# Kernel tuning notes

Measured on AMD Instinct MI355X. Metric: run time of the kernel, lower is better.

The kernel has to match this reference:

```python
import jax, jax.numpy as jnp
import numpy as np

HEADS, DH, M_LAND, PINV_ITERS, LN_EPS = 8, 64, 256, 6, 1e-5


def layer_norm(x, g, b):
    mu = x.mean(-1, keepdims=True)
    var = ((x - mu) ** 2).mean(-1, keepdims=True)
    return (x - mu) * jax.lax.rsqrt(var + LN_EPS) * g + b


def moore_penrose_pinv(x, iters=PINV_ITERS):
    # x: (h, m, m). Iterative Newton-Schulz style pinv (lucidrains).
    abs_x = jnp.abs(x)
    col = abs_x.sum(-1)
    row = abs_x.sum(-2)
    z = jnp.swapaxes(x, -1, -2) / (jnp.max(col) * jnp.max(row))
    I = jnp.eye(x.shape[-1], dtype=x.dtype)
    for _ in range(iters):
        xz = x @ z
        z = 0.25 * z @ (13.0 * I - xz @ (15.0 * I - xz @ (7.0 * I - xz)))
    return z


def nystrom_attention(x, qkv_w, out_w, out_b, res_w):
    # x: (n, dim). No mask, eval mode (dropout off).
    n, dim = x.shape
    pad = (-n) % M_LAND
    xp = jnp.pad(x, ((pad, 0), (0, 0)))  # pad at sequence START, as in original
    n_p = n + pad
    l = n_p // M_LAND  # tokens per landmark
    qkv = xp @ qkv_w  # (n_p, 3*h*dh)
    q, k, v = jnp.split(qkv, 3, axis=-1)
    split = lambda t: t.reshape(n_p, HEADS, DH).transpose(1, 0, 2)  # (h, n_p, dh)
    q, k, v = split(q), split(k), split(v)
    q = q * (DH ** -0.5)
    q_l = q.reshape(HEADS, M_LAND, l, DH).mean(axis=2)  # (h, m, dh)
    k_l = k.reshape(HEADS, M_LAND, l, DH).mean(axis=2)
    sim1 = jnp.einsum('hid,hjd->hij', q, k_l)    # (h, n_p, m)
    sim2 = jnp.einsum('hid,hjd->hij', q_l, k_l)  # (h, m, m)
    sim3 = jnp.einsum('hid,hjd->hij', q_l, k)    # (h, m, n_p)
    a1 = jax.nn.softmax(sim1, axis=-1)
    a2 = jax.nn.softmax(sim2, axis=-1)
    a3 = jax.nn.softmax(sim3, axis=-1)
    a2_inv = moore_penrose_pinv(a2)
    out = a1 @ (a2_inv @ (a3 @ v))  # (h, n_p, dh)
    # residual depthwise conv over sequence dim, kernel 33, per head
    res = jax.lax.conv_general_dilated(
        v[None], res_w, (1, 1), ((16, 16), (0, 0)),
        feature_group_count=HEADS, dimension_numbers=('NCHW', 'OIHW', 'NCHW'))[0]
    out = out + res
    out = out.transpose(1, 0, 2).reshape(n_p, HEADS * DH)
    out = out @ out_w + out_b
    return out[-n:]  # drop the leading pad


def ppeg(x, w7, b7, w5, b5, w3, b3, H, W):
    cls_tok, feat = x[0], x[1:]
    C = feat.shape[1]
    img = feat.T.reshape(1, C, H, W)
    def dw(w, b, p):
        y = jax.lax.conv_general_dilated(
            img, w, (1, 1), ((p, p), (p, p)),
            feature_group_count=C, dimension_numbers=('NCHW', 'OIHW', 'NCHW'))
        return y + b.reshape(1, C, 1, 1)
    out = img + dw(w7, b7, 3) + dw(w5, b5, 2) + dw(w3, b3, 1)
    out = out[0].reshape(C, H * W).T
    return jnp.concatenate([cls_tok[None], out], axis=0)


def forward(h, fc1_w, fc1_b, cls_token, l1_ln_g, l1_ln_b, l1_qkv_w, l1_out_w, l1_out_b, l1_res_w,
            conv7_w, conv7_b, conv5_w, conv5_b, conv3_w, conv3_b,
            l2_ln_g, l2_ln_b, l2_qkv_w, l2_out_w, l2_out_b, l2_res_w,
            norm_g, norm_b, fc2_w, fc2_b):
    x = jax.nn.relu(h @ fc1_w + fc1_b)  # (N, 512)
    N = x.shape[0]
    Hs = Ws = int(np.ceil(np.sqrt(N)))  # N chosen perfect square -> add_length == 0
    x = jnp.concatenate([cls_token, x], axis=0)  # (N+1, 512)
    x = x + nystrom_attention(layer_norm(x, l1_ln_g, l1_ln_b), l1_qkv_w, l1_out_w, l1_out_b, l1_res_w)
    x = ppeg(x, conv7_w, conv7_b, conv5_w, conv5_b, conv3_w, conv3_b, Hs, Ws)
    x = x + nystrom_attention(layer_norm(x, l2_ln_g, l2_ln_b), l2_qkv_w, l2_out_w, l2_out_b, l2_res_w)
    x = layer_norm(x, norm_g, norm_b)[0]  # cls token readout
    return x @ fc2_w + fc2_b  # (n_classes,)


def setup_inputs() -> dict:
    key = jax.random.key(0)
    ks = jax.random.split(key, 16)
    nrm = lambda k, s, sc=0.02: jax.random.normal(k, s, jnp.float32) * sc
    D = 512
    return {
        'h': jax.random.normal(ks[0], (16384, 2048), jnp.float32),
        'fc1_w': nrm(ks[1], (2048, D)), 'fc1_b': jnp.zeros((D,), jnp.float32),
        'cls_token': nrm(ks[2], (1, D), 1.0),
        'l1_ln_g': jnp.ones((D,), jnp.float32), 'l1_ln_b': jnp.zeros((D,), jnp.float32),
        'l1_qkv_w': nrm(ks[3], (D, 3 * D)),
        'l1_out_w': nrm(ks[4], (D, D)), 'l1_out_b': jnp.zeros((D,), jnp.float32),
        'l1_res_w': nrm(ks[5], (HEADS, 1, 33, 1), 0.05),
        'conv7_w': nrm(ks[6], (D, 1, 7, 7), 0.05), 'conv7_b': jnp.zeros((D,), jnp.float32),
        'conv5_w': nrm(ks[7], (D, 1, 5, 5), 0.05), 'conv5_b': jnp.zeros((D,), jnp.float32),
        'conv3_w': nrm(ks[8], (D, 1, 3, 3), 0.05), 'conv3_b': jnp.zeros((D,), jnp.float32),
        'l2_ln_g': jnp.ones((D,), jnp.float32), 'l2_ln_b': jnp.zeros((D,), jnp.float32),
        'l2_qkv_w': nrm(ks[9], (D, 3 * D)),
        'l2_out_w': nrm(ks[10], (D, D)), 'l2_out_b': jnp.zeros((D,), jnp.float32),
        'l2_res_w': nrm(ks[11], (HEADS, 1, 33, 1), 0.05),
        'norm_g': jnp.ones((D,), jnp.float32), 'norm_b': jnp.zeros((D,), jnp.float32),
        'fc2_w': nrm(ks[12], (D, 2)), 'fc2_b': jnp.zeros((2,), jnp.float32),
    }


def reference(h, fc1_w, fc1_b, cls_token, l1_ln_g, l1_ln_b, l1_qkv_w, l1_out_w, l1_out_b, l1_res_w,
              conv7_w, conv7_b, conv5_w, conv5_b, conv3_w, conv3_b,
              l2_ln_g, l2_ln_b, l2_qkv_w, l2_out_w, l2_out_b, l2_res_w,
              norm_g, norm_b, fc2_w, fc2_b):
    return forward(h, fc1_w, fc1_b, cls_token, l1_ln_g, l1_ln_b, l1_qkv_w, l1_out_w, l1_out_b, l1_res_w,
                   conv7_w, conv7_b, conv5_w, conv5_b, conv3_w, conv3_b,
                   l2_ln_g, l2_ln_b, l2_qkv_w, l2_out_w, l2_out_b, l2_res_w,
                   norm_g, norm_b, fc2_w, fc2_b)
```

## Files before the change

kernel.cpp:

```cpp
#include <hip/hip_runtime.h>
#include <cstddef>

#define NROWS 16385
#define NPAD  16640
#define PADT  255
#define DIM   512
#define HEADS 8
#define DH    64
#define NL    256
#define LCH   65
#define LCHUNK 52
#define KCH   320
#define SLACK 24
#define LDST  40

typedef short bf16x8 __attribute__((ext_vector_type(8)));
typedef float f32x4  __attribute__((ext_vector_type(4)));

__device__ __forceinline__ float wsum(float v){
#pragma unroll
  for (int o = 32; o; o >>= 1) v += __shfl_xor(v, o);
  return v;
}
__device__ __forceinline__ float wmax(float v){
#pragma unroll
  for (int o = 32; o; o >>= 1) v = fmaxf(v, __shfl_xor(v, o));
  return v;
}
__device__ __forceinline__ float red16max(float v){
  v = fmaxf(v, __shfl_xor(v, 1));
  v = fmaxf(v, __shfl_xor(v, 2));
  v = fmaxf(v, __shfl_xor(v, 4));
  v = fmaxf(v, __shfl_xor(v, 8));
  return v;
}
__device__ __forceinline__ float red16sum(float v){
  v += __shfl_xor(v, 1);
  v += __shfl_xor(v, 2);
  v += __shfl_xor(v, 4);
  v += __shfl_xor(v, 8);
  return v;
}

__device__ __forceinline__ void split2(float x, unsigned short &h, unsigned short &l){
  unsigned ux = __float_as_uint(x);
  unsigned rh = (ux + 0x7FFFu + ((ux >> 16) & 1u)) >> 16;
  h = (unsigned short)rh;
  float fh = __uint_as_float(rh << 16);
  float r = x - fh;
  unsigned ur = __float_as_uint(r);
  unsigned rl = (ur + 0x7FFFu + ((ur >> 16) & 1u)) >> 16;
  l = (unsigned short)rl;
}
__device__ __forceinline__ float bf2f(unsigned short h){
  return __uint_as_float((unsigned)h << 16);
}

__global__ __launch_bounds__(256) void gemm64_sp_kernel(
    const unsigned short* __restrict__ Ah, const unsigned short* __restrict__ Al,
    const unsigned short* __restrict__ Bth, const unsigned short* __restrict__ Btl,
    const unsigned short* __restrict__ IBh, const unsigned short* __restrict__ IBl,
    float* __restrict__ Cf,
    unsigned short* __restrict__ Crh, unsigned short* __restrict__ Crl,
    unsigned short* __restrict__ Cth, unsigned short* __restrict__ Ctl,
    int M, int N, int K, long sA, long sB, long sC,
    float alpha, float ib)
{
  size_t zo = (size_t)blockIdx.z;
  Ah  += zo*sA; Al  += zo*sA;
  Bth += zo*sB; Btl += zo*sB;
  if (IBh){ IBh += zo*sA; IBl += zo*sA; }
  if (Cf)  Cf  += zo*sC;
  if (Crh){ Crh += zo*sC; Crl += zo*sC; }
  if (Cth){ Cth += zo*sC; Ctl += zo*sC; }
  __shared__ unsigned short LAh[64*LDST], LAl[64*LDST], LBh[64*LDST], LBl[64*LDST];
  const int t = threadIdx.x;
  const int wid = t >> 6, lane = t & 63;
  const int wr = wid >> 1, wc = wid & 1;
  const int l15 = lane & 15, kb = lane >> 4;
  const int bm = blockIdx.y << 6, bn = blockIdx.x << 6;
  const int r4 = t >> 2, kc = (t & 3) << 3;
  f32x4 acc[2][2];
#pragma unroll
  for (int i=0;i<2;++i)
#pragma unroll
    for (int j=0;j<2;++j) acc[i][j] = (f32x4){0.f,0.f,0.f,0.f};

  for (int k0 = 0; k0 < K; k0 += 32){
    __syncthreads();
    {
      int lo = r4*LDST + kc;
      *(uint4*)&LAh[lo] = *(const uint4*)&Ah[(size_t)(bm+r4)*K + k0 + kc];
      *(uint4*)&LAl[lo] = *(const uint4*)&Al[(size_t)(bm+r4)*K + k0 + kc];
      *(uint4*)&LBh[lo] = *(const uint4*)&Bth[(size_t)(bn+r4)*K + k0 + kc];
      *(uint4*)&LBl[lo] = *(const uint4*)&Btl[(size_t)(bn+r4)*K + k0 + kc];
    }
    __syncthreads();
    bf16x8 ah[2], al[2], bh[2], bl[2];
#pragma unroll
    for (int r=0;r<2;++r){
      int off = (wr*32 + r*16 + l15)*LDST + kb*8;
      ah[r] = *(const bf16x8*)&LAh[off];
      al[r] = *(const bf16x8*)&LAl[off];
    }
#pragma unroll
    for (int c2=0;c2<2;++c2){
      int off = (wc*32 + c2*16 + l15)*LDST + kb*8;
      bh[c2] = *(const bf16x8*)&LBh[off];
      bl[c2] = *(const bf16x8*)&LBl[off];
    }
#pragma unroll
    for (int r=0;r<2;++r)
#pragma unroll
      for (int c2=0;c2<2;++c2){
        acc[r][c2] = __builtin_amdgcn_mfma_f32_16x16x32_bf16(ah[r], bh[c2], acc[r][c2], 0,0,0);
        acc[r][c2] = __builtin_amdgcn_mfma_f32_16x16x32_bf16(ah[r], bl[c2], acc[r][c2], 0,0,0);
        acc[r][c2] = __builtin_amdgcn_mfma_f32_16x16x32_bf16(al[r], bh[c2], acc[r][c2], 0,0,0);
      }
  }
#pragma unroll
  for (int r=0;r<2;++r){
#pragma unroll
    for (int c2=0;c2<2;++c2){
      int col = bn + wc*32 + c2*16 + l15;
      int rb  = bm + wr*32 + r*16 + kb*4;
      float v[4];
#pragma unroll
      for (int e=0;e<4;++e){
        float x = acc[r][c2][e];
        if (ib != 0.f){
          size_t io = (size_t)(rb+e)*K + col;
          float ibv = bf2f(IBh[io]) + bf2f(IBl[io]);
          x = alpha*(ib*ibv - x);
        } else {
          x = alpha*x;
        }
        v[e] = x;
      }
      if (Cf){
#pragma unroll
        for (int e=0;e<4;++e) Cf[(size_t)(rb+e)*N + col] = v[e];
      }
      if (Crh){
#pragma unroll
        for (int e=0;e<4;++e){
          unsigned short hh, ll;
          split2(v[e], hh, ll);
          Crh[(size_t)(rb+e)*N + col] = hh;
          Crl[(size_t)(rb+e)*N + col] = ll;
        }
      }
      if (Cth){
        unsigned short h4[4], l4[4];
#pragma unroll
        for (int e=0;e<4;++e) split2(v[e], h4[e], l4[e]);
        uint2 uh, ul;
        uh.x = (unsigned)h4[0] | ((unsigned)h4[1]<<16);
        uh.y = (unsigned)h4[2] | ((unsigned)h4[3]<<16);
        ul.x = (unsigned)l4[0] | ((unsigned)l4[1]<<16);
        ul.y = (unsigned)l4[2] | ((unsigned)l4[3]<<16);
        *(uint2*)&Cth[(size_t)col*M + rb] = uh;
        *(uint2*)&Ctl[(size_t)col*M + rb] = ul;
      }
    }
  }
}

// ... 93 lines not shown
  const int l15 = lane & 15, kb = lane >> 4;
  const int sr = t >> 1, sc0 = (t & 1) << 4;
  f32x4 acc[4][4];
#pragma unroll
  for (int i=0;i<4;++i)
#pragma unroll
    for (int j=0;j<4;++j) acc[i][j] = (f32x4){0.f,0.f,0.f,0.f};

  for (int k0 = 0; k0 < K; k0 += 32){
    __syncthreads();
    {
      const float* ap = A + (size_t)(bm + sr)*K + k0 + sc0;
      float va[16];
      *(float4*)&va[0]  = ((const float4*)ap)[0];
      *(float4*)&va[4]  = ((const float4*)ap)[1];
      *(float4*)&va[8]  = ((const float4*)ap)[2];
      *(float4*)&va[12] = ((const float4*)ap)[3];
      int lo = sr*LDST + sc0;
      unsigned* dh = (unsigned*)&LAh[lo];
      unsigned* dl = (unsigned*)&LAl[lo];
#pragma unroll
      for (int q=0;q<8;++q){
        unsigned short h0,l0,h1,l1;
        split2(va[2*q],   h0, l0);
        split2(va[2*q+1], h1, l1);
        dh[q] = (unsigned)h0 | ((unsigned)h1 << 16);
        dl[q] = (unsigned)l0 | ((unsigned)l1 << 16);
      }
      size_t gb = (size_t)(bn + sr)*K + k0 + sc0;
      uint4 b0 = *(const uint4*)(BTh + gb);
      uint4 b1 = *(const uint4*)(BTh + gb + 8);
      uint4 b2 = *(const uint4*)(BTl + gb);
      uint4 b3 = *(const uint4*)(BTl + gb + 8);
      *(uint4*)&LBh[lo] = b0; *(uint4*)&LBh[lo+8] = b1;
      *(uint4*)&LBl[lo] = b2; *(uint4*)&LBl[lo+8] = b3;
    }
    __syncthreads();
    bf16x8 ah[4], al[4], bh[4], bl[4];
#pragma unroll
    for (int ai=0; ai<4; ++ai){
      int off = (wr*64 + ai*16 + l15)*LDST + kb*8;
      ah[ai] = *(const bf16x8*)&LAh[off];
      al[ai] = *(const bf16x8*)&LAl[off];
    }
#pragma unroll
    for (int bj=0; bj<4; ++bj){
      int off = (wc*64 + bj*16 + l15)*LDST + kb*8;
      bh[bj] = *(const bf16x8*)&LBh[off];
      bl[bj] = *(const bf16x8*)&LBl[off];
    }
#pragma unroll
    for (int ai=0; ai<4; ++ai)
#pragma unroll
      for (int bj=0; bj<4; ++bj){
        acc[ai][bj] = __builtin_amdgcn_mfma_f32_16x16x32_bf16(ah[ai], bh[bj], acc[ai][bj], 0,0,0);
        acc[ai][bj] = __builtin_amdgcn_mfma_f32_16x16x32_bf16(ah[ai], bl[bj], acc[ai][bj], 0,0,0);
        acc[ai][bj] = __builtin_amdgcn_mfma_f32_16x16x32_bf16(al[ai], bh[bj], acc[ai][bj], 0,0,0);
      }
  }
#pragma unroll
  for (int ai=0; ai<4; ++ai){
#pragma unroll
    for (int bj=0; bj<4; ++bj){
      int col = bn + wc*64 + bj*16 + l15;
      float bv = bias ? bias[col] : 0.f;
#pragma unroll
      for (int r=0; r<4; ++r){
        int row = bm + wr*64 + ai*16 + kb*4 + r;
        float v = acc[ai][bj][r] + bv;
        if (relu) v = fmaxf(v, 0.f);
        C[(size_t)row*N + col] = v;
      }
    }
  }
}

__global__ void wt_split_T_kernel(const float* __restrict__ W,
                                  unsigned short* __restrict__ BTh,
                                  unsigned short* __restrict__ BTl, int K, int N)
{
  int idx = blockIdx.x*256 + threadIdx.x;
  if (idx >= N*K) return;
  int n = idx / K, k = idx - n*K;
  unsigned short h, l;
  split2(W[(size_t)k*N + n], h, l);
  BTh[idx] = h; BTl[idx] = l;
}

__global__ void att_split_kernel(const float* __restrict__ ATT,
                                 unsigned short* __restrict__ Ah,
                                 unsigned short* __restrict__ Al)
{
  size_t i4 = (size_t)blockIdx.x*256 + threadIdx.x;
  size_t e = i4*4;
  int row = (int)(e >> 9);
  float4 v = make_float4(0.f,0.f,0.f,0.f);
  if (row < NROWS) v = *(const float4*)(ATT + (size_t)PADT*DIM + e);
  unsigned short h0,l0,h1,l1,h2,l2,h3,l3;
  split2(v.x,h0,l0); split2(v.y,h1,l1); split2(v.z,h2,l2); split2(v.w,h3,l3);
  uint2 uh, ul;
  uh.x = (unsigned)h0 | ((unsigned)h1<<16); uh.y = (unsigned)h2 | ((unsigned)h3<<16);
  ul.x = (unsigned)l0 | ((unsigned)l1<<16); ul.y = (unsigned)l2 | ((unsigned)l3<<16);
  *(uint2*)(Ah + e) = uh;
  *(uint2*)(Al + e) = ul;
}

__global__ __launch_bounds__(256) void ln_pad_sb_kernel(
    const float* __restrict__ X, const float* __restrict__ g,
    const float* __restrict__ b, unsigned short* __restrict__ Yh,
    unsigned short* __restrict__ Yl)
{
  int p = blockIdx.x;
  int t = threadIdx.x;
  size_t base = (size_t)p*DIM;
  if (p < PADT){
    Yh[base+t] = 0; Yh[base+t+256] = 0;
    Yl[base+t] = 0; Yl[base+t+256] = 0;
    return;
  }
  const float* xr = X + (size_t)(p-PADT)*DIM;
  float x0 = xr[t], x1 = xr[t+256];
  float s = x0 + x1, sq = x0*x0 + x1*x1;
  s = wsum(s); sq = wsum(sq);
  __shared__ float rs[4], rq[4];
  if ((t&63)==0){ rs[t>>6]=s; rq[t>>6]=sq; }
  __syncthreads();
  float S = rs[0]+rs[1]+rs[2]+rs[3];
  float SQ = rq[0]+rq[1]+rq[2]+rq[3];
  float mu = S * (1.f/DIM);
  float var = SQ * (1.f/DIM) - mu*mu;
  float r = rsqrtf(var + 1e-5f);
  float y0 = (x0-mu)*r*g[t]     + b[t];
  float y1 = (x1-mu)*r*g[t+256] + b[t+256];
  unsigned short h, l;
  split2(y0, h, l); Yh[base+t] = h;     Yl[base+t] = l;
  split2(y1, h, l); Yh[base+t+256] = h; Yl[base+t+256] = l;
}

__global__ void landmarks_kernel(const float* __restrict__ QKV,
                                 float* __restrict__ QL, float* __restrict__ KL)
{
  int m = blockIdx.x, h = blockIdx.y, d = threadIdx.x;
  float sq = 0.f, sk = 0.f;
  const float* base = QKV + (size_t)(m*LCH)*1536 + (h<<6) + d;
  for (int j = 0; j < LCH; ++j){
    sq += base[0];
    sk += base[512];
    base += 1536;
  }
  QL[(((h<<8)+m)<<6) + d] = sq * (0.125f/65.f);
  KL[(((h<<8)+m)<<6) + d] = sk * (1.f/65.f);
}

__global__ __launch_bounds__(256) void sim2_kernel(
    const float* __restrict__ QL, const float* __restrict__ KL, float* __restrict__ A2)
{
  int m = blockIdx.x, h = blockIdx.y, n = threadIdx.x;
  __shared__ float ql[64];
  __shared__ float red[4];
  if (n < 64) ql[n] = QL[(((h<<8)+m)<<6) + n];
  __syncthreads();
  const float* kl = KL + (size_t)(((h<<8)+n)<<6);
  float s = 0.f;
#pragma unroll
  for (int d=0; d<64; ++d) s += ql[d]*kl[d];
  float mx = wmax(s);
  if ((n&63)==0) red[n>>6] = mx;
  __syncthreads();
  mx = fmaxf(fmaxf(red[0],red[1]), fmaxf(red[2],red[3]));
  float e = __expf(s - mx);
  float sm = wsum(e);
  __syncthreads();
  if ((n&63)==0) red[n>>6] = sm;
  __syncthreads();
  sm = red[0]+red[1]+red[2]+red[3];
  A2[((size_t)((h<<8)+m)<<8) + n] = e/sm;
}

__global__ void crsum_kernel(const float* __restrict__ A2, float* __restrict__ CR)
{
  int b = blockIdx.x, t = threadIdx.x;
  float v;
  if (b < 2048){
    v = fabsf(A2[((size_t)b<<8) + t]);
  } else {
    int r = b - 2048;
    int h = r >> 8, n = r & 255;
    v = fabsf(A2[((size_t)h<<16) + (t<<8) + n]);
  }
  v = wsum(v);
  __shared__ float red[4];
  if ((t&63)==0) red[t>>6]=v;
  __syncthreads();
  if (t==0) CR[b] = red[0]+red[1]+red[2]+red[3];
}
__global__ void maxprod_kernel(const float* __restrict__ CR, float* __restrict__ SCAL)
{
  int t = threadIdx.x;
  float mc = -3e38f, mr = -3e38f;
  for (int i=t; i<2048; i+=256){ mc = fmaxf(mc, CR[i]); mr = fmaxf(mr, CR[2048+i]); }
  mc = wmax(mc); mr = wmax(mr);
  __shared__ float rc[4], rr[4];
  if ((t&63)==0){ rc[t>>6]=mc; rr[t>>6]=mr; }
  __syncthreads();
  if (t==0){
    float a = fmaxf(fmaxf(rc[0],rc[1]),fmaxf(rc[2],rc[3]));
    float b = fmaxf(fmaxf(rr[0],rr[1]),fmaxf(rr[2],rr[3]));
    SCAL[0] = 1.f/(a*b);
  }
}

__global__ void tsplit_kernel(const float* __restrict__ A2, const float* __restrict__ SCAL,
                              unsigned short* __restrict__ A2h, unsigned short* __restrict__ A2l,
                              unsigned short* __restrict__ Zrh, unsigned short* __restrict__ Zrl,
                              unsigned short* __restrict__ Zth, unsigned short* __restrict__ Ztl)
{
  int idx = blockIdx.x*256 + threadIdx.x;
  int h = idx >> 16, rem = idx & 65535, m = rem >> 8, n = rem & 255;
  float a = A2[idx];
  unsigned short hh, ll;
  split2(a, hh, ll);
  A2h[idx] = hh; A2l[idx] = ll;
  float z = a * SCAL[0];
  split2(z, hh, ll);
  Zth[idx] = hh; Ztl[idx] = ll;
  size_t rmo = ((size_t)h<<16) + (n<<8) + m;
  Zrh[rmo] = hh; Zrl[rmo] = ll;
}

__global__ __launch_bounds__(256) void lattn2_kernel(
    const float* __restrict__ QKV, const float* __restrict__ QL,
    float* __restrict__ PACC, float* __restrict__ PML)
{
  const int c = blockIdx.x, lg = blockIdx.y, h = blockIdx.z;
  const int t = threadIdx.x, tx = t & 15, ty = t >> 4;
  __shared__ float QLs[64][68], KtsPs[64][68], Vs[64][68];
  {
    int r = t >> 2, c0 = (t & 3) << 4;
    const float* src = QL + (((size_t)((h << 8) + (lg << 6) + r)) << 6) + c0;
#pragma unroll
    for (int q = 0; q < 4; ++q)
      *(float4*)&QLs[r][c0 + (q<<2)] = ((const float4*)src)[q];
  }
  float M[4], L[4], acc[4][4];
#pragma unroll
  for (int i = 0; i < 4; ++i){
    M[i] = -3e38f; L[i] = 0.f;
#pragma unroll
    for (int j = 0; j < 4; ++j) acc[i][j] = 0.f;
  }
  const int key = t & 63, kd0 = (t >> 6) << 4;
  const int vr = t >> 2, vc = (t & 3) << 4;
  for (int s = 0; s < 5; ++s){
    const int j0 = c * KCH + (s << 6);
    __syncthreads();
    {
      const float* kp = QKV + (size_t)(j0 + key) * 1536 + 512 + (h << 6) + kd0;
#pragma unroll
      for (int q = 0; q < 4; ++q){
        float4 kv = ((const float4*)kp)[q];
        KtsPs[kd0 + (q<<2) + 0][key] = kv.x;
        KtsPs[kd0 + (q<<2) + 1][key] = kv.y;
        KtsPs[kd0 + (q<<2) + 2][key] = kv.z;
        KtsPs[kd0 + (q<<2) + 3][key] = kv.w;
      }
      const float* vp = QKV + (size_t)(j0 + vr) * 1536 + 1024 + (h << 6) + vc;
#pragma unroll
      for (int q = 0; q < 4; ++q)
        *(float4*)&Vs[vr][vc + (q<<2)] = ((const float4*)vp)[q];
    }
    __syncthreads();
    float sv[4][4];
#pragma unroll
    for (int i=0;i<4;++i)
#pragma unroll
      for (int j=0;j<4;++j) sv[i][j] = 0.f;
    for (int d = 0; d < 64; d += 4){
      float a[4][4], b[4][4];
#pragma unroll
      for (int i = 0; i < 4; ++i)
        *(float4*)a[i] = *(const float4*)&QLs[(ty<<2)+i][d];
#pragma unroll
      for (int dd = 0; dd < 4; ++dd)
        *(float4*)b[dd] = *(const float4*)&KtsPs[d+dd][tx<<2];
#pragma unroll
      for (int i = 0; i < 4; ++i)
#pragma unroll
        for (int dd = 0; dd < 4; ++dd){
          float av = a[i][dd];
#pragma unroll
          for (int j = 0; j < 4; ++j) sv[i][j] += av * b[dd][j];
        }
    }
#pragma unroll
    for (int i = 0; i < 4; ++i){
      float rm = fmaxf(fmaxf(sv[i][0], sv[i][1]), fmaxf(sv[i][2], sv[i][3]));
      rm = red16max(rm);
      float Mn = fmaxf(M[i], rm);
      float sc = __expf(M[i] - Mn);
      float rs = 0.f;
#pragma unroll
      for (int j = 0; j < 4; ++j){
        float p = __expf(sv[i][j] - Mn);
        sv[i][j] = p; rs += p;
      }
      rs = red16sum(rs);
      L[i] = L[i] * sc + rs;
      M[i] = Mn;
#pragma unroll
      for (int j = 0; j < 4; ++j) acc[i][j] *= sc;
    }
    __syncthreads();
#pragma unroll
    for (int i = 0; i < 4; ++i)
      *(float4*)&KtsPs[(ty<<2)+i][tx<<2] = *(float4*)sv[i];
    for (int k = 0; k < 64; k += 4){
      float a[4][4], b[4][4];
#pragma unroll
      for (int i = 0; i < 4; ++i)
        *(float4*)a[i] = *(const float4*)&KtsPs[(ty<<2)+i][k];
#pragma unroll
      for (int kk = 0; kk < 4; ++kk)
        *(float4*)b[kk] = *(const float4*)&Vs[k+kk][tx<<2];
#pragma unroll
      for (int i = 0; i < 4; ++i)
#pragma unroll
        for (int kk = 0; kk < 4; ++kk){
          float av = a[i][kk];
#pragma unroll
          for (int j = 0; j < 4; ++j) acc[i][j] += av * b[kk][j];
        }
    }
  }
  size_t base = (size_t)(c * 8 + h) * 256 + (lg << 6) + (ty << 2);
#pragma unroll
  for (int i = 0; i < 4; ++i)
    *(float4*)&PACC[(base + i) * 64 + (tx << 2)] = *(float4*)acc[i];
  if (tx == 0){
#pragma unroll
    for (int i = 0; i < 4; ++i){
      PML[(base + i) * 2 + 0] = M[i];
      PML[(base + i) * 2 + 1] = L[i];
    }
  }
}

__global__ void lattn_combine_kernel(const float* __restrict__ PACC,
                                     const float* __restrict__ PML,
                                     unsigned short* __restrict__ TMth,
                                     unsigned short* __restrict__ TMtl)
{
  int hm = blockIdx.x, d = threadIdx.x;
  int h = hm >> 8, m = hm & 255;
  float Mg = -3e38f;
#pragma unroll
  for (int c = 0; c < LCHUNK; ++c){
    size_t b = ((size_t)(c * 8 + h) * 256 + m) * 2;
    Mg = fmaxf(Mg, PML[b]);
  }
  float Sg = 0.f, o = 0.f;
#pragma unroll 4
  for (int c = 0; c < LCHUNK; ++c){
    size_t b = ((size_t)(c * 8 + h) * 256 + m) * 2;
    float e = __expf(PML[b] - Mg);
    Sg += PML[b+1] * e;
    o += PACC[((size_t)(c * 8 + h) * 256 + m) * 64 + d] * e;
  }
  unsigned short hh, ll;
  split2(o / Sg, hh, ll);
  size_t off = (size_t)h*16384 + (size_t)d*256 + m;
  TMth[off] = hh; TMtl[off] = ll;
}

__global__ __launch_bounds__(256) void attn2_kernel(
    const float* __restrict__ QKV, const float* __restrict__ KL,
    const float* __restrict__ BM, float* __restrict__ ATT)
{
  const int h = blockIdx.y;
  const int t = threadIdx.x;
  const int d0 = (t & 3) << 4;
  const int rp = t >> 2;
  const int row0 = blockIdx.x*128 + rp*2;
  __shared__ float KLs[64][64];
  __shared__ float BMs[64][64];
  float q[2][16], acc[2][16];
  float m[2] = {-3e38f, -3e38f}, l[2] = {0.f, 0.f};
#pragma unroll
  for (int r = 0; r < 2; ++r){
    int qr = row0 + r; if (qr > NROWS-1) qr = NROWS-1;
    const float4* qp = (const float4*)(QKV + (size_t)(PADT+qr)*1536 + (h<<6) + d0);
#pragma unroll
    for (int i = 0; i < 4; ++i){
      float4 v = qp[i];
      q[r][4*i+0]=v.x*0.125f; q[r][4*i+1]=v.y*0.125f;
      q[r][4*i+2]=v.z*0.125f; q[r][4*i+3]=v.w*0.125f;
      acc[r][4*i+0]=0.f; acc[r][4*i+1]=0.f; acc[r][4*i+2]=0.f; acc[r][4*i+3]=0.f;
    }
  }
  for (int c = 0; c < 4; ++c){
    __syncthreads();
    {
      const float4* ks = (const float4*)(KL + (((size_t)(h<<8) + (c<<6))<<6));
      const float4* bs = (const float4*)(BM + ((size_t)h<<14) + ((size_t)(c<<6)<<6));
      float4* kd = (float4*)&KLs[0][0];
      float4* bd = (float4*)&BMs[0][0];
      for (int i = t; i < 1024; i += 256){ kd[i] = ks[i]; bd[i] = bs[i]; }
    }
    __syncthreads();
#pragma unroll 1
    for (int n = 0; n < 64; ++n){
      const float* klr = &KLs[n][d0];
      float sA = 0.f, sB = 0.f;
#pragma unroll
      for (int j = 0; j < 16; ++j){
        sA = fmaf(q[0][j], klr[j], sA);
        sB = fmaf(q[1][j], klr[j], sB);
      }
      sA += __shfl_xor(sA, 1); sA += __shfl_xor(sA, 2);
      sB += __shfl_xor(sB, 1); sB += __shfl_xor(sB, 2);
      const float* bmr = &BMs[n][d0];
      if (sA > m[0]){
        float sc = __expf(m[0] - sA); l[0] *= sc;
#pragma unroll
        for (int j = 0; j < 16; ++j) acc[0][j] *= sc;
        m[0] = sA;
      }
      if (sB > m[1]){
        float sc = __expf(m[1] - sB); l[1] *= sc;
#pragma unroll
        for (int j = 0; j < 16; ++j) acc[1][j] *= sc;
        m[1] = sB;
      }
      float pA = __expf(sA - m[0]); l[0] += pA;
      float pB = __expf(sB - m[1]); l[1] += pB;
#pragma unroll
      for (int j = 0; j < 16; ++j){
        acc[0][j] = fmaf(pA, bmr[j], acc[0][j]);
        acc[1][j] = fmaf(pB, bmr[j], acc[1][j]);
      }
    }
  }
#pragma unroll
  for (int r = 0; r < 2; ++r){
    int row = row0 + r;
    if (row < NROWS){
      float inv = 1.f/l[r];
      float* op = ATT + (size_t)(PADT+row)*DIM + (h<<6) + d0;
#pragma unroll
      for (int j = 0; j < 16; j += 4){
        float4 o;
        o.x=acc[r][j]*inv; o.y=acc[r][j+1]*inv; o.z=acc[r][j+2]*inv; o.w=acc[r][j+3]*inv;
        *(float4*)(op+j) = o;
      }
    }
  }
}

__global__ void zero_slack_kernel(float* __restrict__ QKV)
{
  int i = blockIdx.x*256 + threadIdx.x;
  QKV[(size_t)NPAD*1536 + i] = 0.f;
}

__global__ __launch_bounds__(256) void convres2_kernel(
    const float* __restrict__ QKV, const float* __restrict__ rw,
    float* __restrict__ ATT)
{
  const int t = threadIdx.x;
  const int c = blockIdx.y*256 + t;
  const int i0 = PADT + (blockIdx.x << 2);
  const int h = c >> 6;
  float w[33];
#pragma unroll
  for (int k=0;k<33;++k) w[k] = rw[h*33 + k];
  float acc[4] = {0.f,0.f,0.f,0.f};
  const float* vbase = QKV + (size_t)(i0-16)*1536 + 1024 + c;
#pragma unroll
  for (int rr=0; rr<36; ++rr){
    float v = vbase[(size_t)rr*1536];
#pragma unroll
    for (int k=0;k<4;++k){
      int tap = rr - k;
      if (tap >= 0 && tap <= 32) acc[k] += w[tap]*v;
    }
  }
#pragma unroll
  for (int k=0;k<4;++k){
    int i = i0 + k;
    if (i < NPAD) ATT[(size_t)i*DIM + c] += acc[k];
  }
}

__global__ void pad_kernel(const float* __restrict__ X, float* __restrict__ PIM)
{
  int r = blockIdx.x;
  int c = blockIdx.y*256 + threadIdx.x;
  int py = r / 134, px = r - py*134;
  float v = 0.f;
  if (py>=3 && py<131 && px>=3 && px<131)
    v = X[(size_t)(1 + (py-3)*128 + (px-3))*512 + c];
  PIM[(size_t)r*512 + c] = v;
}

__global__ void wtrans_kernel(const float* __restrict__ w7, const float* __restrict__ w5,
                              const float* __restrict__ w3, float* __restrict__ W7T,
                              float* __restrict__ W5T, float* __restrict__ W3T)
{
  int i = blockIdx.x;
  int c = blockIdx.y*256 + threadIdx.x;
  if (i < 49)      W7T[i*512+c]      = w7[c*49+i];
  else if (i < 74) W5T[(i-49)*512+c] = w5[c*25+(i-49)];
  else             W3T[(i-74)*512+c] = w3[c*9+(i-74)];
}

__global__ __launch_bounds__(256) void ppeg2_kernel(
    const float* __restrict__ PIM, const float* __restrict__ W7T,
    const float* __restrict__ W5T, const float* __restrict__ W3T,
    const float* __restrict__ b7, const float* __restrict__ b5,
    const float* __restrict__ b3, float* __restrict__ X2)
{
  const int t = threadIdx.x;
  const int c = blockIdx.z*256 + t;
  const int x = blockIdx.x;
  const int y0 = blockIdx.y << 2;
  float w7r[49], w5r[25], w3r[9];
#pragma unroll
  for (int i=0;i<49;++i) w7r[i] = W7T[i*512 + c];
#pragma unroll
  for (int i=0;i<25;++i) w5r[i] = W5T[i*512 + c];
#pragma unroll
  for (int i=0;i<9;++i)  w3r[i] = W3T[i*512 + c];
  const float bsum = b7[c] + b5[c] + b3[c];
  float acc[4] = {bsum, bsum, bsum, bsum};
  const float* base = PIM + ((size_t)(y0*134 + x))*512 + c;
#pragma unroll
  for (int rr=0; rr<10; ++rr){
#pragma unroll
    for (int cc=0; cc<7; ++cc){
      float v = base[(size_t)(rr*134 + cc)*512];
#pragma unroll
      for (int k=0;k<4;++k){
        const int dy = rr - k - 3, dx = cc - 3;
        if (dy >= -3 && dy <= 3){
          acc[k] += w7r[(dy+3)*7 + (dx+3)] * v;
          if (dy >= -2 && dy <= 2 && dx >= -2 && dx <= 2)
            acc[k] += w5r[(dy+2)*5 + (dx+2)] * v;
          if (dy >= -1 && dy <= 1 && dx >= -1 && dx <= 1)
            acc[k] += w3r[(dy+1)*3 + (dx+1)] * v;
          if (dy == 0 && dx == 0) acc[k] += v;
        }
      }
    }
  }
#pragma unroll
  for (int k=0;k<4;++k)
    X2[(size_t)(1 + (y0+k)*128 + x)*512 + c] = acc[k];
}

__global__ void copy_row_kernel(const float* __restrict__ src, float* __restrict__ dst)
{
  dst[threadIdx.x] = src[threadIdx.x];
}

__global__ void final_kernel(const float* __restrict__ X, const float* __restrict__ g,
                             const float* __restrict__ b, const float* __restrict__ fw,
                             const float* __restrict__ fb, float* __restrict__ out)
{
  int t = threadIdx.x;
  float x0 = X[t], x1 = X[t+256];
  float s = x0 + x1, sq = x0*x0 + x1*x1;
  s = wsum(s); sq = wsum(sq);
  __shared__ float rs[4], rq[4];
  if ((t&63)==0){ rs[t>>6]=s; rq[t>>6]=sq; }
  __syncthreads();
  float S = rs[0]+rs[1]+rs[2]+rs[3];
  float SQ = rq[0]+rq[1]+rq[2]+rq[3];
  float mu = S*(1.f/DIM);
  float var = SQ*(1.f/DIM) - mu*mu;
  float r = rsqrtf(var + 1e-5f);
  float n0 = (x0-mu)*r*g[t]     + b[t];
  float n1 = (x1-mu)*r*g[t+256] + b[t+256];
  float p0 = n0*fw[t*2]   + n1*fw[(t+256)*2];
  float p1 = n0*fw[t*2+1] + n1*fw[(t+256)*2+1];
  p0 = wsum(p0); p1 = wsum(p1);
  __shared__ float r0[4], r1[4];
  if ((t&63)==0){ r0[t>>6]=p0; r1[t>>6]=p1; }
  __syncthreads();
  if (t==0){
    out[0] = r0[0]+r0[1]+r0[2]+r0[3] + fb[0];
    out[1] = r1[0]+r1[1]+r1[2]+r1[3] + fb[1];
  }
}

struct Bufs {
  float *Y, *QKV, *QL, *KL, *A2, *CR, *SCAL, *BM, *PACC, *PML, *W7T, *W5T, *W3T;
  unsigned short *Yh, *Yl, *ATh, *ATl, *qBTh, *qBTl, *oBTh, *oBTl, *fBTh, *fBTl;
  unsigned short *A2h, *A2l, *XZrh, *XZrl, *XZth, *XZtl, *Wth, *Wtl, *W2th, *W2tl;
  unsigned short *Z0rh, *Z0rl, *Z0th, *Z0tl, *Z1rh, *Z1rl, *Z1th, *Z1tl;
  unsigned short *TMth, *TMtl;
};

static void attention_layer(float* X, const float* ln_g, const float* ln_b,
                            const float* qkv_w, const float* out_w, const float* out_b,
                            const float* res_w, Bufs& bf, hipStream_t stream)
{
  const long SP = 65536;
  wt_split_T_kernel<<<(1536*512)/256, 256, 0, stream>>>(qkv_w, bf.qBTh, bf.qBTl, 512, 1536);
  wt_split_T_kernel<<<(512*512)/256, 256, 0, stream>>>(out_w, bf.oBTh, bf.oBTl, 512, 512);
  ln_pad_sb_kernel<<<NPAD, 256, 0, stream>>>(X, ln_g, ln_b, bf.Yh, bf.Yl);
  gemm_sb_kernel<<<dim3(12,130),256,0,stream>>>(bf.Yh, bf.Yl, bf.qBTh, bf.qBTl,
      nullptr, bf.QKV, NPAD, 1536, 512, 0);
  landmarks_kernel<<<dim3(NL,HEADS),64,0,stream>>>(bf.QKV, bf.QL, bf.KL);
  sim2_kernel<<<dim3(NL,HEADS),256,0,stream>>>(bf.QL, bf.KL, bf.A2);
  crsum_kernel<<<4096,256,0,stream>>>(bf.A2, bf.CR);
  maxprod_kernel<<<1,256,0,stream>>>(bf.CR, bf.SCAL);
  tsplit_kernel<<<2048,256,0,stream>>>(bf.A2, bf.SCAL, bf.A2h, bf.A2l,
      bf.Z0rh, bf.Z0rl, bf.Z0th, bf.Z0tl);
  unsigned short *Zarh=bf.Z0rh, *Zarl=bf.Z0rl, *Zath=bf.Z0th, *Zatl=bf.Z0tl;
  unsigned short *Zbrh=bf.Z1rh, *Zbrl=bf.Z1rl, *Zbth=bf.Z1th, *Zbtl=bf.Z1tl;
  for (int it = 0; it < 6; ++it){
    gemm64_sp_kernel<<<dim3(4,4,8),256,0,stream>>>(bf.A2h, bf.A2l, Zath, Zatl,
        nullptr, nullptr, nullptr, bf.XZrh, bf.XZrl, bf.XZth, bf.XZtl,
        256,256,256, SP,SP,SP, 1.f, 0.f);
    gemm64_sp_kernel<<<dim3(4,4,8),256,0,stream>>>(bf.XZrh, bf.XZrl, bf.XZth, bf.XZtl,
        bf.XZrh, bf.XZrl, nullptr, nullptr, nullptr, bf.Wth, bf.Wtl,
        256,256,256, SP,SP,SP, 1.f, 7.f);
    gemm64_sp_kernel<<<dim3(4,4,8),256,0,stream>>>(bf.XZrh, bf.XZrl, bf.Wth, bf.Wtl,
        bf.XZrh, bf.XZrl, nullptr, nullptr, nullptr, bf.W2th, bf.W2tl,
        256,256,256, SP,SP,SP, 1.f, 15.f);
    gemm64_sp_kernel<<<dim3(4,4,8),256,0,stream>>>(Zarh, Zarl, bf.W2th, bf.W2tl,
        Zarh, Zarl, nullptr, Zbrh, Zbrl, Zbth, Zbtl,
        256,256,256, SP,SP,SP, 0.25f, 13.f);
    unsigned short* tp;
    tp=Zarh; Zarh=Zbrh; Zbrh=tp;  tp=Zarl; Zarl=Zbrl; Zbrl=tp;
    tp=Zath; Zath=Zbth; Zbth=tp;  tp=Zatl; Zatl=Zbtl; Zbtl=tp;
  }
  lattn2_kernel<<<dim3(LCHUNK,4,HEADS),256,0,stream>>>(bf.QKV, bf.QL, bf.PACC, bf.PML);
  lattn_combine_kernel<<<2048,64,0,stream>>>(bf.PACC, bf.PML, bf.TMth, bf.TMtl);
  gemm64_sp_kernel<<<dim3(1,4,8),256,0,stream>>>(Zarh, Zarl, bf.TMth, bf.TMtl,
      nullptr, nullptr, bf.BM, nullptr, nullptr, nullptr, nullptr,
      256,64,256, SP, 16384L, 16384L, 1.f, 0.f);
  float* ATT = bf.Y;
  attn2_kernel<<<dim3(129,HEADS),256,0,stream>>>(bf.QKV, bf.KL, bf.BM, ATT);
  convres2_kernel<<<dim3(4097,2),256,0,stream>>>(bf.QKV, res_w, ATT);
  att_split_kernel<<<8256,256,0,stream>>>(ATT, bf.ATh, bf.ATl);
  gemm_sb_kernel<<<dim3(4,129),256,0,stream>>>(bf.ATh, bf.ATl, bf.oBTh, bf.oBTl,
      out_b, X, NROWS, 512, 512, 1);
}

extern "C" void kernel_launch(void* const* d_in, const int* in_sizes, int n_in,
                              void* d_out, int out_size, void* d_ws, size_t ws_size,
                              hipStream_t stream)
{
  (void)in_sizes; (void)n_in; (void)out_size; (void)ws_size;
  const float* h       = (const float*)d_in[0];
  const float* fc1_w   = (const float*)d_in[1];
  const float* fc1_b   = (const float*)d_in[2];
  const float* cls     = (const float*)d_in[3];
  const float* l1_ln_g = (const float*)d_in[4];
  const float* l1_ln_b = (const float*)d_in[5];
  const float* l1_qkv_w= (const float*)d_in[6];
  const float* l1_out_w= (const float*)d_in[7];
  const float* l1_out_b= (const float*)d_in[8];
  const float* l1_res_w= (const float*)d_in[9];
  const float* conv7_w = (const float*)d_in[10];
  const float* conv7_b = (const float*)d_in[11];
  const float* conv5_w = (const float*)d_in[12];
  const float* conv5_b = (const float*)d_in[13];
  const float* conv3_w = (const float*)d_in[14];
  const float* conv3_b = (const float*)d_in[15];
  const float* l2_ln_g = (const float*)d_in[16];
  const float* l2_ln_b = (const float*)d_in[17];
  const float* l2_qkv_w= (const float*)d_in[18];
  const float* l2_out_w= (const float*)d_in[19];
  const float* l2_out_b= (const float*)d_in[20];
  const float* l2_res_w= (const float*)d_in[21];
  const float* norm_g  = (const float*)d_in[22];
  const float* norm_b  = (const float*)d_in[23];
  const float* fc2_w   = (const float*)d_in[24];
  const float* fc2_b   = (const float*)d_in[25];

  float* ws = (float*)d_ws;
  float* X   = ws;                 ws += (size_t)NROWS*DIM;
  float* X2  = ws;                 ws += (size_t)NROWS*DIM;
  Bufs bf;
  bf.Y    = ws;                    ws += (size_t)NPAD*DIM;
  bf.QKV  = ws;                    ws += (size_t)(NPAD+SLACK)*1536;
  bf.QL   = ws;                    ws += HEADS*NL*DH;
  bf.KL   = ws;                    ws += HEADS*NL*DH;
  bf.A2   = ws;                    ws += HEADS*NL*NL;
  bf.CR   = ws;                    ws += 4096;
  bf.SCAL = ws;                    ws += 8;
  bf.BM   = ws;                    ws += HEADS*NL*DH;
  bf.PACC = ws;                    ws += (size_t)LCHUNK*HEADS*NL*DH;
  bf.PML  = ws;                    ws += (size_t)LCHUNK*HEADS*NL*2;
  bf.W7T  = ws;                    ws += 49*512;
  bf.W5T  = ws;                    ws += 25*512;
  bf.W3T  = ws;                    ws += 9*512;
  unsigned short* us = (unsigned short*)ws;
  bf.Yh   = us;                    us += (size_t)NPAD*DIM;
  bf.Yl   = us;                    us += (size_t)NPAD*DIM;
  bf.ATh  = us;                    us += (size_t)16512*DIM;
  bf.ATl  = us;                    us += (size_t)16512*DIM;
  bf.qBTh = us;                    us += 1536*512;
  bf.qBTl = us;                    us += 1536*512;
  bf.oBTh = us;                    us += 512*512;
  bf.oBTl = us;                    us += 512*512;
  bf.fBTh = us;                    us += 512*2048;
  bf.fBTl = us;                    us += 512*2048;
  const size_t PL = (size_t)HEADS*NL*NL;
  bf.A2h  = us; us += PL;  bf.A2l  = us; us += PL;
  bf.XZrh = us; us += PL;  bf.XZrl = us; us += PL;
  bf.XZth = us; us += PL;  bf.XZtl = us; us += PL;
  bf.Wth  = us; us += PL;  bf.Wtl  = us; us += PL;
  bf.W2th = us; us += PL;  bf.W2tl = us; us += PL;
  bf.Z0rh = us; us += PL;  bf.Z0rl = us; us += PL;
  bf.Z0th = us; us += PL;  bf.Z0tl = us; us += PL;
  bf.Z1rh = us; us += PL;  bf.Z1rl = us; us += PL;
  bf.Z1th = us; us += PL;  bf.Z1tl = us; us += PL;
  bf.TMth = us; us += (size_t)HEADS*NL*DH;
  bf.TMtl = us; us += (size_t)HEADS*NL*DH;
  float* PIM = bf.QKV;

  zero_slack_kernel<<<(SLACK*1536)/256, 256, 0, stream>>>(bf.QKV);
  wtrans_kernel<<<dim3(83,2),256,0,stream>>>(conv7_w, conv5_w, conv3_w,
                                             bf.W7T, bf.W5T, bf.W3T);

  wt_split_T_kernel<<<(512*2048)/256, 256, 0, stream>>>(fc1_w, bf.fBTh, bf.fBTl, 2048, 512);
  gemm_sbf_kernel<<<dim3(4,128),256,0,stream>>>(h, bf.fBTh, bf.fBTl, fc1_b, X + DIM,
      16384, 512, 2048, 1);
  copy_row_kernel<<<1,512,0,stream>>>(cls, X);

  attention_layer(X, l1_ln_g, l1_ln_b, l1_qkv_w, l1_out_w, l1_out_b, l1_res_w, bf, stream);

  pad_kernel<<<dim3(17956,2),256,0,stream>>>(X, PIM);
  ppeg2_kernel<<<dim3(128,32,2),256,0,stream>>>(PIM, bf.W7T, bf.W5T, bf.W3T,
                                                conv7_b, conv5_b, conv3_b, X2);
  copy_row_kernel<<<1,512,0,stream>>>(X, X2);

  attention_layer(X2, l2_ln_g, l2_ln_b, l2_qkv_w, l2_out_w, l2_out_b, l2_res_w, bf, stream);

  final_kernel<<<1,256,0,stream>>>(X2, norm_g, norm_b, fc2_w, fc2_b, (float*)d_out);
}
```

Baseline: 2.302 ms.

## Move attn1 landmark attention onto split-bf16 MFMA with online softmax

Replaces the scalar FP32 a1·(pinv·a3v) attention kernel with an MFMA version. Q, landmark keys and the BM matrix are split into bf16 hi/lo pairs, and three MFMAs per product emulate fp32 accuracy. A new kernel pre-splits KL, and the gemm now emits BM transposed and split. The aim is to cut the FP32 ALU cost of the per-row 256-landmark softmax-attention, at the price of extra LDS staging, more syncs and an extra small kernel launch.

```diff
diff --git a/kernel.cpp b/kernel.cpp
--- a/kernel.cpp
+++ b/kernel.cpp
@@ -13,6 +13,7 @@
 #define KCH   320
 #define SLACK 24
 #define LDST  40
+#define AST   72
 
 typedef short bf16x8 __attribute__((ext_vector_type(8)));
 typedef float f32x4  __attribute__((ext_vector_type(4)));
@@ -412,6 +413,16 @@
   KL[(((h<<8)+m)<<6) + d] = sk * (1.f/65.f);
 }
 
+__global__ void klsplit_kernel(const float* __restrict__ KL,
+                               unsigned short* __restrict__ KLh,
+                               unsigned short* __restrict__ KLl)
+{
+  int i = blockIdx.x*256 + threadIdx.x;
+  unsigned short h, l;
+  split2(KL[i], h, l);
+  KLh[i] = h; KLl[i] = l;
+}
+
 __global__ __launch_bounds__(256) void sim2_kernel(
     const float* __restrict__ QL, const float* __restrict__ KL, float* __restrict__ A2)
 {
@@ -632,86 +643,158 @@
   TMth[off] = hh; TMtl[off] = ll;
 }
 
-__global__ __launch_bounds__(256) void attn2_kernel(
-    const float* __restrict__ QKV, const float* __restrict__ KL,
-    const float* __restrict__ BM, float* __restrict__ ATT)
-{
-  const int h = blockIdx.y;
+__global__ __launch_bounds__(256) void attn3_kernel(
+    const float* __restrict__ QKV,
+    const unsigned short* __restrict__ KLh, const unsigned short* __restrict__ KLl,
+    const unsigned short* __restrict__ BMth, const unsigned short* __restrict__ BMtl,
+    float* __restrict__ ATT)
+{
+  const int qb = blockIdx.x, h = blockIdx.y;
   const int t = threadIdx.x;
-  const int d0 = (t & 3) << 4;
-  const int rp = t >> 2;
-  const int row0 = blockIdx.x*128 + rp*2;
-  __shared__ float KLs[64][64];
-  __shared__ float BMs[64][64];
-  float q[2][16], acc[2][16];
-  float m[2] = {-3e38f, -3e38f}, l[2] = {0.f, 0.f};
-#pragma unroll
-  for (int r = 0; r < 2; ++r){
-    int qr = row0 + r; if (qr > NROWS-1) qr = NROWS-1;
-    const float4* qp = (const float4*)(QKV + (size_t)(PADT+qr)*1536 + (h<<6) + d0);
-#pragma unroll
-    for (int i = 0; i < 4; ++i){
-      float4 v = qp[i];
-      q[r][4*i+0]=v.x*0.125f; q[r][4*i+1]=v.y*0.125f;
-      q[r][4*i+2]=v.z*0.125f; q[r][4*i+3]=v.w*0.125f;
-      acc[r][4*i+0]=0.f; acc[r][4*i+1]=0.f; acc[r][4*i+2]=0.f; acc[r][4*i+3]=0.f;
-    }
-  }
-  for (int c = 0; c < 4; ++c){
+  const int w = t >> 6, lane = t & 63;
+  const int l15 = lane & 15, kb = lane >> 4;
+  __shared__ unsigned short LQh[64*AST], LQl[64*AST];
+  __shared__ unsigned short LAh[64*AST], LAl[64*AST];
+  __shared__ unsigned short LPh[64*AST], LPl[64*AST];
+  {
+    int r = t >> 2, kc = (t & 3) << 4;
+    int row = qb*64 + r; if (row > NROWS-1) row = NROWS-1;
+    const float* qp = QKV + (size_t)(PADT+row)*1536 + (h<<6) + kc;
+    float va[16];
+    *(float4*)&va[0]  = ((const float4*)qp)[0];
+    *(float4*)&va[4]  = ((const float4*)qp)[1];
+    *(float4*)&va[8]  = ((const float4*)qp)[2];
+    *(float4*)&va[12] = ((const float4*)qp)[3];
+    unsigned* dh = (unsigned*)&LQh[r*AST + kc];
+    unsigned* dl = (unsigned*)&LQl[r*AST + kc];
+#pragma unroll
+    for (int q=0;q<8;++q){
+      unsigned short h0,l0,h1,l1;
+      split2(va[2*q]*0.125f,   h0, l0);
+      split2(va[2*q+1]*0.125f, h1, l1);
+      dh[q] = (unsigned)h0 | ((unsigned)h1 << 16);
+      dl[q] = (unsigned)l0 | ((unsigned)l1 << 16);
+    }
+  }
+  float m = -3e38f, l = 0.f;
+  f32x4 oacc[4];
+#pragma unroll
+  for (int i=0;i<4;++i) oacc[i] = (f32x4){0.f,0.f,0.f,0.f};
+  const int sr = t >> 2, sc0 = (t & 3) << 4;
+
+  for (int lt = 0; lt < 4; ++lt){
     __syncthreads();
     {
-      const float4* ks = (const float4*)(KL + (((size_t)(h<<8) + (c<<6))<<6));
-      const float4* bs = (const float4*)(BM + ((size_t)h<<14) + ((size_t)(c<<6)<<6));
-      float4* kd = (float4*)&KLs[0][0];
-      float4* bd = (float4*)&BMs[0][0];
-      for (int i = t; i < 1024; i += 256){ kd[i] = ks[i]; bd[i] = bs[i]; }
-    }
-    __syncthreads();
-#pragma unroll 1
-    for (int n = 0; n < 64; ++n){
-      const float* klr = &KLs[n][d0];
-      float sA = 0.f, sB = 0.f;
-#pragma unroll
-      for (int j = 0; j < 16; ++j){
-        sA = fmaf(q[0][j], klr[j], sA);
-        sB = fmaf(q[1][j], klr[j], sB);
-      }
-      sA += __shfl_xor(sA, 1); sA += __shfl_xor(sA, 2);
-      sB += __shfl_xor(sB, 1); sB += __shfl_xor(sB, 2);
-      const float* bmr = &BMs[n][d0];
-      if (sA > m[0]){
-        float sc = __expf(m[0] - sA); l[0] *= sc;
-#pragma unroll
-        for (int j = 0; j < 16; ++j) acc[0][j] *= sc;
-        m[0] = sA;
-      }
-      if (sB > m[1]){
-        float sc = __expf(m[1] - sB); l[1] *= sc;
-#pragma unroll
-        for (int j = 0; j < 16; ++j) acc[1][j] *= sc;
-        m[1] = sB;
-      }
-      float pA = __expf(sA - m[0]); l[0] += pA;
-      float pB = __expf(sB - m[1]); l[1] += pB;
-#pragma unroll
-      for (int j = 0; j < 16; ++j){
-        acc[0][j] = fmaf(pA, bmr[j], acc[0][j]);
-        acc[1][j] = fmaf(pB, bmr[j], acc[1][j]);
-      }
-    }
-  }
-#pragma unroll
-  for (int r = 0; r < 2; ++r){
-    int row = row0 + r;
-    if (row < NROWS){
-      float inv = 1.f/l[r];
-      float* op = ATT + (size_t)(PADT+row)*DIM + (h<<6) + d0;
-#pragma unroll
-      for (int j = 0; j < 16; j += 4){
-        float4 o;
-        o.x=acc[r][j]*inv; o.y=acc[r][j+1]*inv; o.z=acc[r][j+2]*inv; o.w=acc[r][j+3]*inv;
-        *(float4*)(op+j) = o;
-      }
+      size_t g = ((size_t)(h*256 + lt*64 + sr))*64 + sc0;
+      uint4 vh0 = *(const uint4*)&KLh[g];
+      uint4 vh1 = *(const uint4*)&KLh[g+8];
+      uint4 vl0 = *(const uint4*)&KLl[g];
+      uint4 vl1 = *(const uint4*)&KLl[g+8];
+      int lo = sr*AST + sc0;
+      *(uint4*)&LAh[lo]   = vh0;
+      *(uint4*)&LAh[lo+8] = vh1;
+      *(uint4*)&LAl[lo]   = vl0;
+      *(uint4*)&LAl[lo+8] = vl1;
+    }
+    __syncthreads();
+    f32x4 sacc[4];
+#pragma unroll
+    for (int i=0;i<4;++i) sacc[i] = (f32x4){0.f,0.f,0.f,0.f};
+#pragma unroll
+    for (int ks = 0; ks < 2; ++ks){
+      int qoff = (w*16 + l15)*AST + ks*32 + kb*8;
+      bf16x8 bh = *(const bf16x8*)&LQh[qoff];
+      bf16x8 bl = *(const bf16x8*)&LQl[qoff];
+#pragma unroll
+      for (int mi=0; mi<4; ++mi){
+        int aoff = (mi*16 + l15)*AST + ks*32 + kb*8;
+        bf16x8 ah = *(const bf16x8*)&LAh[aoff];
+        bf16x8 al = *(const bf16x8*)&LAl[aoff];
+        sacc[mi] = __builtin_amdgcn_mfma_f32_16x16x32_bf16(ah, bh, sacc[mi], 0,0,0);
+        sacc[mi] = __builtin_amdgcn_mfma_f32_16x16x32_bf16(ah, bl, sacc[mi], 0,0,0);
+        sacc[mi] = __builtin_amdgcn_mfma_f32_16x16x32_bf16(al, bh, sacc[mi], 0,0,0);
+      }
+    }
+    float tm = -3e38f;
+#pragma unroll
+    for (int mi=0;mi<4;++mi)
+#pragma unroll
+      for (int e=0;e<4;++e) tm = fmaxf(tm, sacc[mi][e]);
+    tm = fmaxf(tm, __shfl_xor(tm, 16));
+    tm = fmaxf(tm, __shfl_xor(tm, 32));
+    float Mn = fmaxf(m, tm);
+    float sc = __expf(m - Mn);
+    float ts = 0.f;
+    float p[4][4];
+#pragma unroll
+    for (int mi=0;mi<4;++mi)
+#pragma unroll
+      for (int e=0;e<4;++e){
+        float pv = __expf(sacc[mi][e] - Mn);
+        p[mi][e] = pv; ts += pv;
+      }
+    ts += __shfl_xor(ts, 16);
+    ts += __shfl_xor(ts, 32);
+    l = l*sc + ts;
+    m = Mn;
+#pragma unroll
+    for (int mi=0;mi<4;++mi)
+#pragma unroll
+      for (int e=0;e<4;++e) oacc[mi][e] *= sc;
+#pragma unroll
+    for (int mi=0;mi<4;++mi){
+      unsigned short h4[4], l4[4];
+#pragma unroll
+      for (int e=0;e<4;++e) split2(p[mi][e], h4[e], l4[e]);
+      uint2 uh, ul;
+      uh.x = (unsigned)h4[0] | ((unsigned)h4[1]<<16);
+      uh.y = (unsigned)h4[2] | ((unsigned)h4[3]<<16);
+      ul.x = (unsigned)l4[0] | ((unsigned)l4[1]<<16);
+      ul.y = (unsigned)l4[2] | ((unsigned)l4[3]<<16);
+      int po = (w*16 + l15)*AST + mi*16 + kb*4;
+      *(uint2*)&LPh[po] = uh;
+      *(uint2*)&LPl[po] = ul;
+    }
+    __syncthreads();
+    {
+      size_t g = ((size_t)(h*64 + sr))*256 + lt*64 + sc0;
+      uint4 vh0 = *(const uint4*)&BMth[g];
+      uint4 vh1 = *(const uint4*)&BMth[g+8];
+      uint4 vl0 = *(const uint4*)&BMtl[g];
+      uint4 vl1 = *(const uint4*)&BMtl[g+8];
+      int lo = sr*AST + sc0;
+      *(uint4*)&LAh[lo]   = vh0;
+      *(uint4*)&LAh[lo+8] = vh1;
+      *(uint4*)&LAl[lo]   = vl0;
+      *(uint4*)&LAl[lo+8] = vl1;
+    }
+    __syncthreads();
+#pragma unroll
+    for (int ks = 0; ks < 2; ++ks){
+      int poff = (w*16 + l15)*AST + ks*32 + kb*8;
+      bf16x8 pbh = *(const bf16x8*)&LPh[poff];
+      bf16x8 pbl = *(const bf16x8*)&LPl[poff];
+#pragma unroll
+      for (int mi=0; mi<4; ++mi){
+        int aoff = (mi*16 + l15)*AST + ks*32 + kb*8;
+        bf16x8 ah = *(const bf16x8*)&LAh[aoff];
+        bf16x8 al = *(const bf16x8*)&LAl[aoff];
+        oacc[mi] = __builtin_amdgcn_mfma_f32_16x16x32_bf16(ah, pbh, oacc[mi], 0,0,0);
+        oacc[mi] = __builtin_amdgcn_mfma_f32_16x16x32_bf16(ah, pbl, oacc[mi], 0,0,0);
+        oacc[mi] = __builtin_amdgcn_mfma_f32_16x16x32_bf16(al, pbh, oacc[mi], 0,0,0);
+      }
+    }
+  }
+  int row = qb*64 + w*16 + l15;
+  if (row < NROWS){
+    float inv = 1.f / l;
+    float* op = ATT + (size_t)(PADT+row)*DIM + (h<<6) + kb*4;
+#pragma unroll
+    for (int mi=0;mi<4;++mi){
+      float4 o;
+      o.x = oacc[mi][0]*inv; o.y = oacc[mi][1]*inv;
+      o.z = oacc[mi][2]*inv; o.w = oacc[mi][3]*inv;
+      *(float4*)(op + mi*16) = o;
     }
   }
 }
@@ -853,11 +936,11 @@
 }
 
 struct Bufs {
-  float *Y, *QKV, *QL, *KL, *A2, *CR, *SCAL, *BM, *PACC, *PML, *W7T, *W5T, *W3T;
+  float *Y, *QKV, *QL, *KL, *A2, *CR, *SCAL, *PACC, *PML, *W7T, *W5T, *W3T;
   unsigned short *Yh, *Yl, *ATh, *ATl, *qBTh, *qBTl, *oBTh, *oBTl, *fBTh, *fBTl;
   unsigned short *A2h, *A2l, *XZrh, *XZrl, *XZth, *XZtl, *Wth, *Wtl, *W2th, *W2tl;
   unsigned short *Z0rh, *Z0rl, *Z0th, *Z0tl, *Z1rh, *Z1rl, *Z1th, *Z1tl;
-  unsigned short *TMth, *TMtl;
+  unsigned short *TMth, *TMtl, *KLh, *KLl, *BMth, *BMtl;
 };
 
 static void attention_layer(float* X, const float* ln_g, const float* ln_b,
@@ -871,6 +954,7 @@
   gemm_sb_kernel<<<dim3(12,130),256,0,stream>>>(bf.Yh, bf.Yl, bf.qBTh, bf.qBTl,
       nullptr, bf.QKV, NPAD, 1536, 512, 0);
   landmarks_kernel<<<dim3(NL,HEADS),64,0,stream>>>(bf.QKV, bf.QL, bf.KL);
+  klsplit_kernel<<<512,256,0,stream>>>(bf.KL, bf.KLh, bf.KLl);
   sim2_kernel<<<dim3(NL,HEADS),256,0,stream>>>(bf.QL, bf.KL, bf.A2);
   crsum_kernel<<<4096,256,0,stream>>>(bf.A2, bf.CR);
   maxprod_kernel<<<1,256,0,stream>>>(bf.CR, bf.SCAL);
@@ -898,10 +982,11 @@
   lattn2_kernel<<<dim3(LCHUNK,4,HEADS),256,0,stream>>>(bf.QKV, bf.QL, bf.PACC, bf.PML);
   lattn_combine_kernel<<<2048,64,0,stream>>>(bf.PACC, bf.PML, bf.TMth, bf.TMtl);
   gemm64_sp_kernel<<<dim3(1,4,8),256,0,stream>>>(Zarh, Zarl, bf.TMth, bf.TMtl,
-      nullptr, nullptr, bf.BM, nullptr, nullptr, nullptr, nullptr,
+      nullptr, nullptr, nullptr, nullptr, nullptr, bf.BMth, bf.BMtl,
       256,64,256, SP, 16384L, 16384L, 1.f, 0.f);
   float* ATT = bf.Y;
-  attn2_kernel<<<dim3(129,HEADS),256,0,stream>>>(bf.QKV, bf.KL, bf.BM, ATT);
+  attn3_kernel<<<dim3(257,HEADS),256,0,stream>>>(bf.QKV, bf.KLh, bf.KLl,
+      bf.BMth, bf.BMtl, ATT);
   convres2_kernel<<<dim3(4097,2),256,0,stream>>>(bf.QKV, res_w, ATT);
   att_split_kernel<<<8256,256,0,stream>>>(ATT, bf.ATh, bf.ATl);
   gemm_sb_kernel<<<dim3(4,129),256,0,stream>>>(bf.ATh, bf.ATl, bf.oBTh, bf.oBTl,
@@ -951,7 +1036,6 @@
   bf.A2   = ws;                    ws += HEADS*NL*NL;
   bf.CR   = ws;                    ws += 4096;
   bf.SCAL = ws;                    ws += 8;
-  bf.BM   = ws;                    ws += HEADS*NL*DH;
   bf.PACC = ws;                    ws += (size_t)LCHUNK*HEADS*NL*DH;
   bf.PML  = ws;                    ws += (size_t)LCHUNK*HEADS*NL*2;
   bf.W7T  = ws;                    ws += 49*512;
@@ -980,6 +1064,10 @@
   bf.Z1th = us; us += PL;  bf.Z1tl = us; us += PL;
   bf.TMth = us; us += (size_t)HEADS*NL*DH;
   bf.TMtl = us; us += (size_t)HEADS*NL*DH;
+  bf.KLh  = us; us += (size_t)HEADS*NL*DH;
+  bf.KLl  = us; us += (size_t)HEADS*NL*DH;
+  bf.BMth = us; us += (size_t)HEADS*NL*DH;
+  bf.BMtl = us; us += (size_t)HEADS*NL*DH;
   float* PIM = bf.QKV;
 
   zero_slack_kernel<<<(SLACK*1536)/256, 256, 0, stream>>>(bf.QKV);
```

After: 2.038 ms. 11.5% less time.
